# Kernel optimization log

Measured on AMD Instinct MI355X. Metric: run time of the kernel, lower is better.

## Reference

```python
import jax, jax.numpy as jnp
import numpy as np

B, S, HID, HEADS, FF, NL, SPAN, MAXP, VOCAB = 8, 512, 512, 8, 768, 3, 256, 512, 100
DH = HID // HEADS
EPS = 1e-7  # layer_norm_eps
SCALE = float(np.sqrt(DH * 3.0))  # scale_factor = 1 + len(['p2c','c2p']) = 3


def _ln(x, s, b):
    mu = x.mean(-1, keepdims=True)
    var = ((x - mu) ** 2).mean(-1, keepdims=True)
    return (x - mu) / jnp.sqrt(var + EPS) * s + b


def _rel_bucket(seq_len, bucket=SPAN, max_pos=MAXP):
    # DeBERTa-v2 build_relative_position + make_log_bucket_position (static, numpy)
    ids = np.arange(seq_len)
    rel = ids[:, None] - ids[None, :]
    mid = bucket // 2
    abs_pos = np.where((rel < mid) & (rel > -mid), mid - 1, np.abs(rel)).astype(np.float64)
    log_pos = np.ceil(np.log(abs_pos / mid) / np.log((max_pos - 1) / mid) * (mid - 1)) + mid
    bucket_pos = np.where(abs_pos <= mid, rel.astype(np.float64), log_pos * np.sign(rel))
    return jnp.asarray(bucket_pos.astype(np.int32))  # [S, S]


def setup_inputs():
    key = jax.random.key(0)
    ks = jax.random.split(key, 12)
    w = lambda k, shape: jax.random.normal(k, shape, jnp.float32) * 0.02
    return {
        'image_embeddings': jax.random.normal(ks[0], (B, S, HID), jnp.float32),
        'attention_mask': jnp.ones((B, S), jnp.float32),
        'emb_ln_s': jnp.ones((HID,), jnp.float32), 'emb_ln_b': jnp.zeros((HID,), jnp.float32),
        'rel_emb': w(ks[1], (2 * SPAN, HID)),
        'rel_ln_s': jnp.ones((HID,), jnp.float32), 'rel_ln_b': jnp.zeros((HID,), jnp.float32),
        'Wq': w(ks[2], (NL, HID, HID)), 'bq': jnp.zeros((NL, HID), jnp.float32),
        'Wk': w(ks[3], (NL, HID, HID)), 'bk': jnp.zeros((NL, HID), jnp.float32),
        'Wv': w(ks[4], (NL, HID, HID)), 'bv': jnp.zeros((NL, HID), jnp.float32),
        'Wo': w(ks[5], (NL, HID, HID)), 'bo': jnp.zeros((NL, HID), jnp.float32),
        'attn_ln_s': jnp.ones((NL, HID), jnp.float32), 'attn_ln_b': jnp.zeros((NL, HID), jnp.float32),
        'Wi': w(ks[6], (NL, HID, FF)), 'bi': jnp.zeros((NL, FF), jnp.float32),
        'Wf': w(ks[7], (NL, FF, HID)), 'bf': jnp.zeros((NL, HID), jnp.float32),
        'ffn_ln_s': jnp.ones((NL, HID), jnp.float32), 'ffn_ln_b': jnp.zeros((NL, HID), jnp.float32),
        'Wc': w(ks[8], (HID, VOCAB)), 'bc': jnp.zeros((VOCAB,), jnp.float32),
    }


def reference(image_embeddings, attention_mask, emb_ln_s, emb_ln_b, rel_emb, rel_ln_s, rel_ln_b,
              Wq, bq, Wk, bk, Wv, bv, Wo, bo, attn_ln_s, attn_ln_b,
              Wi, bi, Wf, bf, ffn_ln_s, ffn_ln_b, Wc, bc):
    b, s, hid = image_embeddings.shape
    rel = _rel_bucket(s)
    c2p_idx = jnp.clip(rel + SPAN, 0, 2 * SPAN - 1)[None, None]   # [1,1,S,S]
    p2c_idx = jnp.clip(-rel + SPAN, 0, 2 * SPAN - 1)[None, None]  # [1,1,S,S]

    # embeddings: LayerNorm(inputs_embeds) * mask (position_biased_input=False)
    h = _ln(image_embeddings, emb_ln_s, emb_ln_b) * attention_mask[:, :, None]
    rel_e = _ln(rel_emb, rel_ln_s, rel_ln_b)  # norm_rel_ebd='layer_norm'
    m = (attention_mask[:, None, :, None] * attention_mask[:, None, None, :]) > 0  # [B,1,S,S]
    neg = jnp.finfo(h.dtype).min

    for l in range(NL):
        q = (h @ Wq[l] + bq[l]).reshape(b, s, HEADS, DH)
        k = (h @ Wk[l] + bk[l]).reshape(b, s, HEADS, DH)
        v = (h @ Wv[l] + bv[l]).reshape(b, s, HEADS, DH)
        scores = jnp.einsum('bqhd,bkhd->bhqk', q, k) / SCALE
        # share_att_key=True: pos projections reuse key/query projections
        pk = (rel_e @ Wk[l] + bk[l]).reshape(2 * SPAN, HEADS, DH)
        pq = (rel_e @ Wq[l] + bq[l]).reshape(2 * SPAN, HEADS, DH)
        # content-to-position
        c2p = jnp.einsum('bqhd,rhd->bhqr', q, pk)  # [B,H,S,2*SPAN]
        c2p = jnp.take_along_axis(c2p, c2p_idx, axis=-1)  # [B,H,S,S]
        # position-to-content (gather along last dim, then transpose q/k)
        p2c = jnp.einsum('bkhd,rhd->bhkr', k, pq)  # [B,H,S,2*SPAN]
        p2c = jnp.take_along_axis(p2c, p2c_idx, axis=-1).transpose(0, 1, 3, 2)  # [B,H,S,S]
        scores = scores + c2p / SCALE + p2c / SCALE
        # XSoftmax: mask -> -inf, softmax, re-zero masked probs
        probs = jax.nn.softmax(jnp.where(m, scores, neg), axis=-1)
        probs = jnp.where(m, probs, 0.0)
        ctx = jnp.einsum('bhqk,bkhd->bqhd', probs, v).reshape(b, s, hid)
        h = _ln(ctx @ Wo[l] + bo[l] + h, attn_ln_s[l], attn_ln_b[l])
        f = jax.nn.gelu(h @ Wi[l] + bi[l], approximate=False)
        h = _ln(f @ Wf[l] + bf[l] + h, ffn_ln_s[l], ffn_ln_b[l])

    return h @ Wc + bc  # token-classification logits [B,S,VOCAB]
```

## Files before the change

### kernel.cpp

```cpp
#include <hip/hip_runtime.h>
#include <hip/hip_bf16.h>
#include <math.h>

#define EPS_LN 1e-7f
#define INV_SCALE 0.072168783648703221f
#define NEGMAX -3.402823466e38f

typedef unsigned short u16;
typedef __attribute__((ext_vector_type(8))) short bf16x8;
typedef __attribute__((ext_vector_type(4))) float f32x4;

__device__ __forceinline__ u16 f2b(float f) {
  union { float f; unsigned int u; } v; v.f = f;
  unsigned int r = v.u + 0x7FFFu + ((v.u >> 16) & 1u);
  return (u16)(r >> 16);
}
__device__ __forceinline__ float b2f(u16 u) {
  union { unsigned int u; float f; } v; v.u = ((unsigned int)u) << 16;
  return v.f;
}
__device__ __forceinline__ float gelu_exact(float v) {
  return 0.5f * v * (1.f + erff(v * 0.70710678118654752440f));
}
__device__ __forceinline__ int bucket_clip(int rel) {
  int a = (rel < 128 && rel > -128) ? 127 : (rel < 0 ? -rel : rel);
  int bucket;
  if (a <= 128) {
    bucket = rel;
  } else {
    double lp = ceil(log((double)a / 128.0) / log(511.0 / 128.0) * 127.0) + 128.0;
    int l = (int)lp;
    bucket = (rel > 0) ? l : -l;
  }
  int c = bucket + 256;
  return c < 0 ? 0 : (c > 511 ? 511 : c);
}

__global__ __launch_bounds__(256) void relbucket_kernel(int* __restrict__ crel) {
  int idx = blockIdx.x * 256 + threadIdx.x;
  if (idx >= 1023) return;
  crel[idx] = bucket_clip(idx - 511);
}

__global__ __launch_bounds__(256) void biascat_kernel(const float* __restrict__ bq,
                                                      const float* __restrict__ bk,
                                                      const float* __restrict__ bv,
                                                      float* __restrict__ o) {
  int i = blockIdx.x * 256 + threadIdx.x;
  if (i >= 4608) return;
  int l = i / 1536, c = i - l * 1536;
  float v = (c < 512) ? bq[l * 512 + c]
                      : (c < 1024) ? bk[l * 512 + c - 512] : bv[l * 512 + c - 1024];
  o[i] = v;
}

template <bool RESID, bool MASK>
__global__ __launch_bounds__(256) void ln_kernel(const float* __restrict__ x,
                                                 const float* __restrict__ res,
                                                 const float* __restrict__ gam,
                                                 const float* __restrict__ bet,
                                                 const float* __restrict__ mask,
                                                 float* __restrict__ out,
                                                 u16* __restrict__ outb, int nrows) {
  int w = threadIdx.x >> 6, ln = threadIdx.x & 63;
  int row = blockIdx.x * 4 + w;
  if (row >= nrows) return;
  const float* xr = x + (size_t)row * 512;
  float v[8];
#pragma unroll
  for (int c = 0; c < 2; ++c) {
    float4 a = *(const float4*)(xr + (ln << 3) + (c << 2));
    v[c * 4 + 0] = a.x; v[c * 4 + 1] = a.y; v[c * 4 + 2] = a.z; v[c * 4 + 3] = a.w;
    if (RESID) {
      float4 r4 = *(const float4*)(res + (size_t)row * 512 + (ln << 3) + (c << 2));
      v[c * 4 + 0] += r4.x; v[c * 4 + 1] += r4.y; v[c * 4 + 2] += r4.z; v[c * 4 + 3] += r4.w;
    }
  }
  float sum = 0.f;
#pragma unroll
  for (int c = 0; c < 8; ++c) sum += v[c];
#pragma unroll
  for (int off = 32; off; off >>= 1) sum += __shfl_xor(sum, off);
  float mu = sum * (1.f / 512.f);
  float vs = 0.f;
#pragma unroll
  for (int c = 0; c < 8; ++c) { float d = v[c] - mu; vs += d * d; }
#pragma unroll
  for (int off = 32; off; off >>= 1) vs += __shfl_xor(vs, off);
  float rstd = 1.f / sqrtf(vs * (1.f / 512.f) + EPS_LN);
  float mk = MASK ? mask[row] : 1.f;
  float* orow = out + (size_t)row * 512;
  u16* brow = outb ? outb + (size_t)row * 512 : nullptr;
#pragma unroll
  for (int c = 0; c < 2; ++c) {
    int col = (ln << 3) + (c << 2);
    float o[4];
#pragma unroll
    for (int q = 0; q < 4; ++q)
      o[q] = ((v[c * 4 + q] - mu) * rstd * gam[col + q] + bet[col + q]) * mk;
    *(float4*)(orow + col) = make_float4(o[0], o[1], o[2], o[3]);
    if (brow) {
      ushort4 ob = { f2b(o[0]), f2b(o[1]), f2b(o[2]), f2b(o[3]) };
      *(ushort4*)(brow + col) = ob;
    }
  }
}

__global__ __launch_bounds__(256) void wtrans_kernel(const float* __restrict__ W,
                                                     u16* __restrict__ Wt,
                                                     int K, int N, long wstride, long tstride) {
  __shared__ float tl[32][33];
  int z = blockIdx.z;
  W += (size_t)z * wstride;
  Wt += (size_t)z * tstride;
  int n0 = blockIdx.x * 32, k0 = blockIdx.y * 32;
  int c = threadIdx.x & 31, r8 = threadIdx.x >> 5;
#pragma unroll
  for (int p = 0; p < 4; ++p) {
    int r = r8 + p * 8;
    int k = k0 + r, n = n0 + c;
    tl[r][c] = (k < K && n < N) ? W[(size_t)k * N + n] : 0.f;
  }
  __syncthreads();
#pragma unroll
  for (int p = 0; p < 4; ++p) {
    int r = r8 + p * 8;
    int n = n0 + r, k = k0 + c;
    if (n < N && k < K) Wt[(size_t)n * K + k] = f2b(tl[c][r]);
  }
}

__global__ __launch_bounds__(256) void vtrans_kernel(const u16* __restrict__ qkv,
                                                     u16* __restrict__ vT) {
  __shared__ u16 tl[32][33];
  int z = blockIdx.z;
  int b = z >> 3, h = z & 7;
  int j0 = blockIdx.x * 32, d0 = blockIdx.y * 32;
  int c = threadIdx.x & 31, r8 = threadIdx.x >> 5;
#pragma unroll
  for (int p = 0; p < 4; ++p) {
    int r = r8 + p * 8;
    tl[r][c] = qkv[(size_t)(b * 512 + j0 + r) * 1536 + 1024 + h * 64 + d0 + c];
  }
  __syncthreads();
#pragma unroll
  for (int p = 0; p < 4; ++p) {
    int r = r8 + p * 8;
    vT[(size_t)z * 32768 + (size_t)(d0 + r) * 512 + j0 + c] = tl[c][r];
  }
}

template <int EPI, typename CT>
__global__ __launch_bounds__(256) void gemm128(const u16* __restrict__ A,
                                               const u16* __restrict__ B,
                                               const float* __restrict__ bias,
                                               CT* __restrict__ C,
                                               int M, int N, int K,
                                               int lda, int ldb, int ldc) {
  __shared__ u16 As[128][72];
  __shared__ u16 Bs[64][72];
  int t = threadIdx.x;
  int m0 = blockIdx.y * 128, n0 = blockIdx.x * 64;
  int w = t >> 6, l = t & 63;
  int wr = w >> 1, wc = w & 1, lr = l & 15, kg = l >> 4;
  f32x4 acc[4][2] = {};
  for (int k0 = 0; k0 < K; k0 += 64) {
#pragma unroll
    for (int p = 0; p < 4; ++p) {
      int c = t + (p << 8);
      int row = c >> 3, q = c & 7;
      *(uint4*)(&As[row][q * 8]) =
          *(const uint4*)(A + (size_t)(m0 + row) * lda + k0 + q * 8);
    }
#pragma unroll
    for (int p = 0; p < 2; ++p) {
      int c = t + (p << 8);
      int row = c >> 3, q = c & 7;
      *(uint4*)(&Bs[row][q * 8]) =
          *(const uint4*)(B + (size_t)(n0 + row) * ldb + k0 + q * 8);
    }
    __syncthreads();
#pragma unroll
    for (int s = 0; s < 2; ++s) {
      bf16x8 a[4], bb[2];
#pragma unroll
      for (int m = 0; m < 4; ++m)
        a[m] = *(const bf16x8*)(&As[wr * 64 + m * 16 + lr][kg * 8 + s * 32]);
#pragma unroll
      for (int n = 0; n < 2; ++n)
        bb[n] = *(const bf16x8*)(&Bs[wc * 32 + n * 16 + lr][kg * 8 + s * 32]);
#pragma unroll
      for (int m = 0; m < 4; ++m)
#pragma unroll
        for (int n = 0; n < 2; ++n)
          acc[m][n] = __builtin_amdgcn_mfma_f32_16x16x32_bf16(a[m], bb[n], acc[m][n], 0, 0, 0);
    }
    __syncthreads();
  }
#pragma unroll
  for (int m = 0; m < 4; ++m)
#pragma unroll
    for (int n = 0; n < 2; ++n) {
      int col = n0 + wc * 32 + n * 16 + lr;
      float bv = (EPI >= 1) ? bias[col] : 0.f;
#pragma unroll
      for (int r = 0; r < 4; ++r) {
        int row = m0 + wr * 64 + m * 16 + kg * 4 + r;
        float v = acc[m][n][r] + bv;
        if (EPI == 2) v = gelu_exact(v);
        if constexpr (sizeof(CT) == 2) {
          ((u16*)C)[(size_t)row * ldc + col] = f2b(v);
        } else {
          ((float*)C)[(size_t)row * ldc + col] = v;
        }
      }
    }
}

template <int EPI, typename CT>
__global__ __launch_bounds__(256) void gemm_bf16(const u16* __restrict__ A,
                                                 const u16* __restrict__ B,
                                                 const float* __restrict__ bias,
                                                 CT* __restrict__ C,
                                                 int M, int N, int K,
                                                 int lda, int ldb, int ldc) {
  __shared__ u16 As[64][72];
  __shared__ u16 Bs[64][72];
  int t = threadIdx.x;
  int m0 = blockIdx.y * 64, n0 = blockIdx.x * 64;
  int w = t >> 6, l = t & 63;
  int wr = w >> 1, wc = w & 1, lr = l & 15, kg = l >> 4;
  f32x4 acc[2][2] = {};
  for (int k0 = 0; k0 < K; k0 += 64) {
#pragma unroll
    for (int p = 0; p < 2; ++p) {
      int c = t + (p << 8);
      int row = c >> 3, q = c & 7;
      uint4 av = *(const uint4*)(A + (size_t)(m0 + row) * lda + k0 + q * 8);
      *(uint4*)(&As[row][q * 8]) = av;
      uint4 bv = make_uint4(0u, 0u, 0u, 0u);
      if (n0 + row < N) bv = *(const uint4*)(B + (size_t)(n0 + row) * ldb + k0 + q * 8);
      *(uint4*)(&Bs[row][q * 8]) = bv;
    }
    __syncthreads();
#pragma unroll
    for (int s = 0; s < 2; ++s) {
      bf16x8 a0 = *(const bf16x8*)(&As[wr * 32 + lr][kg * 8 + s * 32]);
      bf16x8 a1 = *(const bf16x8*)(&As[wr * 32 + 16 + lr][kg * 8 + s * 32]);
      bf16x8 b0 = *(const bf16x8*)(&Bs[wc * 32 + lr][kg * 8 + s * 32]);
      bf16x8 b1 = *(const bf16x8*)(&Bs[wc * 32 + 16 + lr][kg * 8 + s * 32]);
      acc[0][0] = __builtin_amdgcn_mfma_f32_16x16x32_bf16(a0, b0, acc[0][0], 0, 0, 0);
      acc[0][1] = __builtin_amdgcn_mfma_f32_16x16x32_bf16(a0, b1, acc[0][1], 0, 0, 0);
      acc[1][0] = __builtin_amdgcn_mfma_f32_16x16x32_bf16(a1, b0, acc[1][0], 0, 0, 0);
      acc[1][1] = __builtin_amdgcn_mfma_f32_16x16x32_bf16(a1, b1, acc[1][1], 0, 0, 0);
    }
    __syncthreads();
  }
#pragma unroll
  for (int m = 0; m < 2; ++m)
#pragma unroll
    for (int n = 0; n < 2; ++n) {
      int col = n0 + wc * 32 + n * 16 + lr;
      if (col < N) {
        float bv = (EPI >= 1) ? bias[col] : 0.f;
#pragma unroll
        for (int r = 0; r < 4; ++r) {
          int row = m0 + wr * 32 + m * 16 + kg * 4 + r;
          float v = acc[m][n][r] + bv;
          if (EPI == 2) v = gelu_exact(v);
          if constexpr (sizeof(CT) == 2) {
            ((u16*)C)[(size_t)row * ldc + col] = f2b(v);
          } else {
            ((float*)C)[(size_t)row * ldc + col] = v;
          }
        }
      }
    }
}

__global__ __launch_bounds__(256) void attn_fused(const u16* __restrict__ qkv,
                                                  const u16* __restrict__ vT,
                                                  const float* __restrict__ mask,
                                                  const int* __restrict__ crel,
                                                  u16* __restrict__ po,
                                                  float* __restrict__ pms) {
  __shared__ u16 ks[64][72];
  __shared__ u16 U1[128][72];
  __shared__ u16 U2[128][72];
  __shared__ u16 crl16[1024];
  int t = threadIdx.x;
  int wg = blockIdx.x;
  int xcd = wg & 7, q = wg >> 3;
  int z = xcd * 8 + (q >> 6);
  int rem = q & 63;
  int it = rem >> 3, js = rem & 7;
  int b = z >> 3, h = z & 7;
  int i0 = it * 64, j0 = js * 64;
  int w = t >> 6, l = t & 63;
  int lr = l & 15, kg = l >> 4;

  int ib = bucket_clip(i0 - j0 - 63);

  for (int c = t; c < 1023; c += 256) crl16[c] = (u16)crel[c];
  for (int c = t; c < 512; c += 256) {
    int row = c >> 3, off = (c & 7) * 8;
    *(uint4*)(&ks[row][off]) =
        *(const uint4*)(qkv + (size_t)(b * 512 + j0 + row) * 1536 + 512 + h * 64 + off);
  }
  for (int c = t; c < 1024; c += 256) {
    int row = c >> 3, off = (c & 7) * 8;
    int rw = ib + row;
    rw = rw > 511 ? 511 : rw;
    const u16* relrow = qkv + (size_t)(4096 + rw) * 1536 + h * 64;
    *(uint4*)(&U1[row][off]) = *(const uint4*)(relrow + 512 + off);
    *(uint4*)(&U2[row][off]) = *(const uint4*)(relrow + off);
  }

  const u16* qrow = qkv + (size_t)(b * 512 + i0 + w * 16 + lr) * 1536 + h * 64;
  bf16x8 qa0 = *(const bf16x8*)(qrow + kg * 8);
  bf16x8 qa1 = *(const bf16x8*)(qrow + kg * 8 + 32);
  __syncthreads();

  f32x4 sc[4];
#pragma unroll
  for (int nf = 0; nf < 4; ++nf) {
    bf16x8 kb0 = *(const bf16x8*)(&ks[nf * 16 + lr][kg * 8]);
    bf16x8 kb1 = *(const bf16x8*)(&ks[nf * 16 + lr][kg * 8 + 32]);
    f32x4 a = {};
    a = __builtin_amdgcn_mfma_f32_16x16x32_bf16(qa0, kb0, a, 0, 0, 0);
    a = __builtin_amdgcn_mfma_f32_16x16x32_bf16(qa1, kb1, a, 0, 0, 0);
    sc[nf] = a;
  }
  f32x4 b1a[8];
#pragma unroll
  for (int f = 0; f < 8; ++f) {
    bf16x8 p0 = *(const bf16x8*)(&U1[f * 16 + lr][kg * 8]);
    bf16x8 p1 = *(const bf16x8*)(&U1[f * 16 + lr][kg * 8 + 32]);
    f32x4 a = {};
    a = __builtin_amdgcn_mfma_f32_16x16x32_bf16(qa0, p0, a, 0, 0, 0);
    a = __builtin_amdgcn_mfma_f32_16x16x32_bf16(qa1, p1, a, 0, 0, 0);
    b1a[f] = a;
  }
  f32x4 b2a[2][4];
#pragma unroll
  for (int g = 0; g < 2; ++g) {
    bf16x8 a0 = *(const bf16x8*)(&U2[w * 32 + g * 16 + lr][kg * 8]);
    bf16x8 a1 = *(const bf16x8*)(&U2[w * 32 + g * 16 + lr][kg * 8 + 32]);
#pragma unroll
    for (int f = 0; f < 4; ++f) {
      bf16x8 kb0 = *(const bf16x8*)(&ks[f * 16 + lr][kg * 8]);
      bf16x8 kb1 = *(const bf16x8*)(&ks[f * 16 + lr][kg * 8 + 32]);
      f32x4 a = {};
      a = __builtin_amdgcn_mfma_f32_16x16x32_bf16(a0, kb0, a, 0, 0, 0);
      a = __builtin_amdgcn_mfma_f32_16x16x32_bf16(a1, kb1, a, 0, 0, 0);
      b2a[g][f] = a;
    }
  }
  __syncthreads();
  u16* b1 = &U1[0][0];
#pragma unroll
  for (int f = 0; f < 8; ++f)
#pragma unroll
    for (int r = 0; r < 4; ++r)
      b1[(w * 16 + kg * 4 + r) * 136 + f * 16 + lr] = f2b(b1a[f][r]);
#pragma unroll
  for (int g = 0; g < 2; ++g)
#pragma unroll
    for (int f = 0; f < 4; ++f)
#pragma unroll
      for (int r = 0; r < 4; ++r)
        U2[w * 32 + g * 16 + kg * 4 + r][f * 16 + lr] = f2b(b2a[g][f][r]);
  __syncthreads();

  bf16x8 vb[4][2];
#pragma unroll
  for (int nf = 0; nf < 4; ++nf) {
    const u16* vrow = vT + (size_t)z * 32768 + (size_t)(nf * 16 + lr) * 512 + j0;
    vb[nf][0] = *(const bf16x8*)(vrow + kg * 8);
    vb[nf][1] = *(const bf16x8*)(vrow + kg * 8 + 32);
  }

  float mi[4], mj[4];
#pragma unroll
  for (int r = 0; r < 4; ++r) mi[r] = mask[b * 512 + i0 + w * 16 + kg * 4 + r];
#pragma unroll
  for (int nf = 0; nf < 4; ++nf) mj[nf] = mask[b * 512 + j0 + nf * 16 + lr];
  float lgv[4][4];
  bool ok[4][4];
  float tmax[4] = {NEGMAX, NEGMAX, NEGMAX, NEGMAX};
  int iloc = w * 16 + kg * 4;
#pragma unroll
  for (int nf = 0; nf < 4; ++nf) {
    int jloc = nf * 16 + lr;
    int relc = i0 + iloc - (j0 + jloc) + 511;
#pragma unroll
    for (int r = 0; r < 4; ++r) {
      int idx = crl16[relc + r] - ib;
      float bias = b2f(b1[(iloc + r) * 136 + idx]) + b2f(U2[idx][jloc]);
      bool o_ = (mi[r] * mj[nf]) > 0.f;
      float v = o_ ? (sc[nf][r] + bias) * INV_SCALE : NEGMAX;
      ok[nf][r] = o_;
      lgv[nf][r] = v;
      tmax[r] = fmaxf(tmax[r], v);
    }
  }
#pragma unroll
  for (int r = 0; r < 4; ++r) {
#pragma unroll
    for (int off = 8; off; off >>= 1) tmax[r] = fmaxf(tmax[r], __shfl_xor(tmax[r], off));
  }
  float tsum[4];
#pragma unroll
  for (int r = 0; r < 4; ++r) {
    float mn = tmax[r];
    float ls = 0.f;
#pragma unroll
    for (int nf = 0; nf < 4; ++nf) {
      float p = ok[nf][r] ? __expf(lgv[nf][r] - mn) : 0.f;
      lgv[nf][r] = p;
      ls += p;
    }
    tsum[r] = ls;
  }
#pragma unroll
  for (int r = 0; r < 4; ++r) {
#pragma unroll
    for (int off = 8; off; off >>= 1) tsum[r] += __shfl_xor(tsum[r], off);
  }
#pragma unroll
  for (int nf = 0; nf < 4; ++nf)
#pragma unroll
    for (int r = 0; r < 4; ++r) ks[w * 16 + kg * 4 + r][nf * 16 + lr] = f2b(lgv[nf][r]);
  bf16x8 pa0 = *(const bf16x8*)(&ks[w * 16 + lr][kg * 8]);
  bf16x8 pa1 = *(const bf16x8*)(&ks[w * 16 + lr][kg * 8 + 32]);
  f32x4 o[4] = {};
#pragma unroll
  for (int nf = 0; nf < 4; ++nf) {
    o[nf] = __builtin_amdgcn_mfma_f32_16x16x32_bf16(pa0, vb[nf][0], o[nf], 0, 0, 0);
    o[nf] = __builtin_amdgcn_mfma_f32_16x16x32_bf16(pa1, vb[nf][1], o[nf], 0, 0, 0);
  }
#pragma unroll
  for (int r = 0; r < 4; ++r) {
    int i = i0 + w * 16 + kg * 4 + r;
    size_t pb = (((size_t)js * 64 + z) * 512 + i) * 64;
#pragma unroll
    for (int nf = 0; nf < 4; ++nf) po[pb + nf * 16 + lr] = f2b(o[nf][r]);
    if (lr == 0) {
      size_t mb = (((size_t)js * 64 + z) * 512 + i) * 2;
      pms[mb + 0] = tmax[r];
      pms[mb + 1] = tsum[r];
    }
  }
}

__global__ __launch_bounds__(256) void merge_kernel(const u16* __restrict__ po,
                                                    const float* __restrict__ pms,
                                                    u16* __restrict__ ctx) {
  int t = threadIdx.x;
  int w = t >> 6, d = t & 63;
  int row = blockIdx.x * 4 + w;
  int z = row >> 9, i = row & 511;
  int b = z >> 3, h = z & 7;
  float mv[8], sv[8], m = NEGMAX;
#pragma unroll
  for (int js = 0; js < 8; ++js) {
    size_t mb = (((size_t)js * 64 + z) * 512 + i) * 2;
    mv[js] = pms[mb + 0];
    sv[js] = pms[mb + 1];
    m = fmaxf(m, mv[js]);
  }
  float o = 0.f, s = 0.f;
#pragma unroll
  for (int js = 0; js < 8; ++js) {
    float wgt = (mv[js] <= -1e37f) ? 0.f : __expf(mv[js] - m);
    o += wgt * b2f(po[(((size_t)js * 64 + z) * 512 + i) * 64 + d]);
    s += wgt * sv[js];
  }
  float r = (s > 0.f) ? o / s : 0.f;
  ctx[(size_t)(b * 512 + i) * 512 + h * 64 + d] = f2b(r);
}

extern "C" void kernel_launch(void* const* d_in, const int* in_sizes, int n_in,
                              void* d_out, int out_size, void* d_ws, size_t ws_size,
                              hipStream_t stream) {
  const float* x       = (const float*)d_in[0];
  const float* mask    = (const float*)d_in[1];
  const float* emb_s   = (const float*)d_in[2];
  const float* emb_b   = (const float*)d_in[3];
  const float* rel_emb = (const float*)d_in[4];
  const float* rel_s   = (const float*)d_in[5];
  const float* rel_b   = (const float*)d_in[6];
  const float* Wq = (const float*)d_in[7];
  const float* bq = (const float*)d_in[8];
  const float* Wk = (const float*)d_in[9];
  const float* bk = (const float*)d_in[10];
  const float* Wv = (const float*)d_in[11];
  const float* bv = (const float*)d_in[12];
  const float* Wo = (const float*)d_in[13];
  const float* bo = (const float*)d_in[14];
  const float* as_ = (const float*)d_in[15];
  const float* ab_ = (const float*)d_in[16];
  const float* Wi = (const float*)d_in[17];
  const float* bi = (const float*)d_in[18];
  const float* Wf = (const float*)d_in[19];
  const float* bf_ = (const float*)d_in[20];
  const float* fs_ = (const float*)d_in[21];
  const float* fb_ = (const float*)d_in[22];
  const float* Wc = (const float*)d_in[23];
  const float* bc = (const float*)d_in[24];
  float* out = (float*)d_out;

  char* p = (char*)d_ws;
  auto alloc = [&](size_t bytes) {
    char* r = p;
    p += (bytes + 255) & ~(size_t)255;
    return r;
  };
  float* hcat = (float*)alloc((size_t)4608 * 512 * 4);
  float* tmpA = (float*)alloc((size_t)4096 * 512 * 4);
  u16* mid  = (u16*)alloc((size_t)4096 * 768 * 2);
  u16* hbf  = (u16*)alloc((size_t)4608 * 512 * 2);
  u16* qkv  = (u16*)alloc((size_t)4608 * 1536 * 2);
  u16* vT   = (u16*)alloc((size_t)64 * 64 * 512 * 2);
  u16* ctxb = (u16*)alloc((size_t)4096 * 512 * 2);
  u16* po   = (u16*)alloc((size_t)8 * 64 * 512 * 64 * 2);
  float* pms = (float*)alloc((size_t)8 * 64 * 512 * 2 * 4);
  u16* WtQKV = (u16*)alloc((size_t)3 * 1536 * 512 * 2);
  u16* WtO  = (u16*)alloc((size_t)3 * 512 * 512 * 2);
  u16* WtI  = (u16*)alloc((size_t)3 * 768 * 512 * 2);
  u16* WtF  = (u16*)alloc((size_t)3 * 512 * 768 * 2);
  u16* WtC  = (u16*)alloc((size_t)100 * 512 * 2);
  float* bqkv = (float*)alloc((size_t)3 * 1536 * 4);
  int* crel = (int*)alloc((size_t)1024 * 4);

  relbucket_kernel<<<4, 256, 0, stream>>>(crel);
  biascat_kernel<<<18, 256, 0, stream>>>(bq, bk, bv, bqkv);
  wtrans_kernel<<<dim3(16, 16, 3), 256, 0, stream>>>(Wq, WtQKV, 512, 512, 262144, 786432);
  wtrans_kernel<<<dim3(16, 16, 3), 256, 0, stream>>>(Wk, WtQKV + 262144, 512, 512, 262144, 786432);
  wtrans_kernel<<<dim3(16, 16, 3), 256, 0, stream>>>(Wv, WtQKV + 524288, 512, 512, 262144, 786432);
  wtrans_kernel<<<dim3(16, 16, 3), 256, 0, stream>>>(Wo, WtO, 512, 512, 262144, 262144);
  wtrans_kernel<<<dim3(24, 16, 3), 256, 0, stream>>>(Wi, WtI, 512, 768, 393216, 393216);
  wtrans_kernel<<<dim3(16, 24, 3), 256, 0, stream>>>(Wf, WtF, 768, 512, 393216, 393216);
  wtrans_kernel<<<dim3(4, 16, 1), 256, 0, stream>>>(Wc, WtC, 512, 100, 0, 0);
  ln_kernel<false, true><<<1024, 256, 0, stream>>>(x, nullptr, emb_s, emb_b, mask,
                                                   hcat, hbf, 4096);
  ln_kernel<false, false><<<128, 256, 0, stream>>>(rel_emb, nullptr, rel_s, rel_b, nullptr,
                                                   hcat + (size_t)4096 * 512,
                                                   hbf + (size_t)4096 * 512, 512);

  for (int l = 0; l < 3; ++l) {
    gemm128<1, u16><<<dim3(24, 36), 256, 0, stream>>>(
        hbf, WtQKV + (size_t)l * 786432, bqkv + l * 1536, qkv,
        4608, 1536, 512, 512, 512, 1536);
    vtrans_kernel<<<dim3(16, 2, 64), 256, 0, stream>>>(qkv, vT);
    attn_fused<<<4096, 256, 0, stream>>>(qkv, vT, mask, crel, po, pms);
    merge_kernel<<<8192, 256, 0, stream>>>(po, pms, ctxb);
    gemm128<1, float><<<dim3(8, 32), 256, 0, stream>>>(
        ctxb, WtO + (size_t)l * 262144, bo + l * 512, tmpA, 4096, 512, 512, 512, 512, 512);
    ln_kernel<true, false><<<1024, 256, 0, stream>>>(tmpA, hcat, as_ + l * 512, ab_ + l * 512,
                                                     nullptr, hcat, hbf, 4096);
    gemm128<2, u16><<<dim3(12, 32), 256, 0, stream>>>(
        hbf, WtI + (size_t)l * 393216, bi + l * 768, mid, 4096, 768, 512, 512, 512, 768);
    gemm128<1, float><<<dim3(8, 32), 256, 0, stream>>>(
        mid, WtF + (size_t)l * 393216, bf_ + l * 512, tmpA, 4096, 512, 768, 768, 768, 512);
    ln_kernel<true, false><<<1024, 256, 0, stream>>>(tmpA, hcat, fs_ + l * 512, fb_ + l * 512,
                                                     nullptr, hcat, hbf, 4096);
  }
  gemm_bf16<1, float><<<dim3(2, 64), 256, 0, stream>>>(
      hbf, WtC, bc, out, 4096, 100, 512, 512, 512, 100);
}
```

Measured before the change: 473.9 us.

## Fuse setup kernels, V-transpose into QKV GEMM, trim attention bias tiles

Merges the bucket-table and bias-concat kernels into one launch and the seven weight-transpose launches into one. The V transpose now happens in the QKV GEMM epilogue, which removes the separate vtrans kernel. In the attention kernel, K fragments are loaded straight into registers instead of shared memory. Only the relative-position rows actually spanned by each tile (F fragments) are loaded and multiplied. Softmax uses exp2 with a prescaled log2e factor, and partial outputs are written in a packed fragment layout that the merge kernel reads back with new indexing. The extra epilogue stores slow the QKV GEMM somewhat, and the lost per-launch overlap costs a little, in exchange for fewer launches and less attention work.

```diff
diff --git a/kernel.cpp b/kernel.cpp
--- a/kernel.cpp
+++ b/kernel.cpp
@@ -36,22 +36,20 @@
   return c < 0 ? 0 : (c > 511 ? 511 : c);
 }
 
-__global__ __launch_bounds__(256) void relbucket_kernel(int* __restrict__ crel) {
-  int idx = blockIdx.x * 256 + threadIdx.x;
-  if (idx >= 1023) return;
-  crel[idx] = bucket_clip(idx - 511);
-}
-
-__global__ __launch_bounds__(256) void biascat_kernel(const float* __restrict__ bq,
-                                                      const float* __restrict__ bk,
-                                                      const float* __restrict__ bv,
-                                                      float* __restrict__ o) {
+__global__ __launch_bounds__(256) void tables_kernel(const float* __restrict__ bq,
+                                                     const float* __restrict__ bk,
+                                                     const float* __restrict__ bv,
+                                                     int* __restrict__ crel,
+                                                     float* __restrict__ bqkv) {
   int i = blockIdx.x * 256 + threadIdx.x;
-  if (i >= 4608) return;
-  int l = i / 1536, c = i - l * 1536;
-  float v = (c < 512) ? bq[l * 512 + c]
-                      : (c < 1024) ? bk[l * 512 + c - 512] : bv[l * 512 + c - 1024];
-  o[i] = v;
+  if (i < 1023) crel[i] = bucket_clip(i - 511);
+  int j = i - 1024;
+  if (j >= 0 && j < 4608) {
+    int l = j / 1536, c = j - l * 1536;
+    float v = (c < 512) ? bq[l * 512 + c]
+                        : (c < 1024) ? bk[l * 512 + c - 512] : bv[l * 512 + c - 1024];
+    bqkv[j] = v;
+  }
 }
 
 template <bool RESID, bool MASK>
@@ -106,14 +104,40 @@
   }
 }
 
-__global__ __launch_bounds__(256) void wtrans_kernel(const float* __restrict__ W,
-                                                     u16* __restrict__ Wt,
-                                                     int K, int N, long wstride, long tstride) {
+__global__ __launch_bounds__(256) void wtrans_all(const float* __restrict__ Wq,
+                                                  const float* __restrict__ Wk,
+                                                  const float* __restrict__ Wv,
+                                                  const float* __restrict__ Wo,
+                                                  const float* __restrict__ Wi,
+                                                  const float* __restrict__ Wf,
+                                                  const float* __restrict__ Wc,
+                                                  u16* __restrict__ WtQKV,
+                                                  u16* __restrict__ WtO,
+                                                  u16* __restrict__ WtI,
+                                                  u16* __restrict__ WtF,
+                                                  u16* __restrict__ WtC) {
   __shared__ float tl[32][33];
-  int z = blockIdx.z;
-  W += (size_t)z * wstride;
-  Wt += (size_t)z * tstride;
+  int job = blockIdx.z;
+  const float* W; u16* Wt; int K, N;
+  if (job < 9) {
+    int l = job / 3, p3 = job % 3;
+    W = (p3 == 0 ? Wq : p3 == 1 ? Wk : Wv) + (size_t)l * 262144;
+    Wt = WtQKV + (size_t)l * 786432 + (size_t)p3 * 262144;
+    K = 512; N = 512;
+  } else if (job < 12) {
+    int l = job - 9; W = Wo + (size_t)l * 262144; Wt = WtO + (size_t)l * 262144;
+    K = 512; N = 512;
+  } else if (job < 15) {
+    int l = job - 12; W = Wi + (size_t)l * 393216; Wt = WtI + (size_t)l * 393216;
+    K = 512; N = 768;
+  } else if (job < 18) {
+    int l = job - 15; W = Wf + (size_t)l * 393216; Wt = WtF + (size_t)l * 393216;
+    K = 768; N = 512;
+  } else {
+    W = Wc; Wt = WtC; K = 512; N = 100;
+  }
   int n0 = blockIdx.x * 32, k0 = blockIdx.y * 32;
+  if (n0 >= N || k0 >= K) return;
   int c = threadIdx.x & 31, r8 = threadIdx.x >> 5;
 #pragma unroll
   for (int p = 0; p < 4; ++p) {
@@ -130,33 +154,14 @@
   }
 }
 
-__global__ __launch_bounds__(256) void vtrans_kernel(const u16* __restrict__ qkv,
-                                                     u16* __restrict__ vT) {
-  __shared__ u16 tl[32][33];
-  int z = blockIdx.z;
-  int b = z >> 3, h = z & 7;
-  int j0 = blockIdx.x * 32, d0 = blockIdx.y * 32;
-  int c = threadIdx.x & 31, r8 = threadIdx.x >> 5;
-#pragma unroll
-  for (int p = 0; p < 4; ++p) {
-    int r = r8 + p * 8;
-    tl[r][c] = qkv[(size_t)(b * 512 + j0 + r) * 1536 + 1024 + h * 64 + d0 + c];
-  }
-  __syncthreads();
-#pragma unroll
-  for (int p = 0; p < 4; ++p) {
-    int r = r8 + p * 8;
-    vT[(size_t)z * 32768 + (size_t)(d0 + r) * 512 + j0 + c] = tl[c][r];
-  }
-}
-
-template <int EPI, typename CT>
+template <int EPI, int VT, typename CT>
 __global__ __launch_bounds__(256) void gemm128(const u16* __restrict__ A,
                                                const u16* __restrict__ B,
                                                const float* __restrict__ bias,
                                                CT* __restrict__ C,
                                                int M, int N, int K,
-                                               int lda, int ldb, int ldc) {
+                                               int lda, int ldb, int ldc,
+                                               u16* __restrict__ vTout) {
   __shared__ u16 As[128][72];
   __shared__ u16 Bs[64][72];
   int t = threadIdx.x;
@@ -203,15 +208,25 @@
     for (int n = 0; n < 2; ++n) {
       int col = n0 + wc * 32 + n * 16 + lr;
       float bv = (EPI >= 1) ? bias[col] : 0.f;
+      int rowb = m0 + wr * 64 + m * 16 + kg * 4;
+      float vv[4];
 #pragma unroll
       for (int r = 0; r < 4; ++r) {
-        int row = m0 + wr * 64 + m * 16 + kg * 4 + r;
         float v = acc[m][n][r] + bv;
         if (EPI == 2) v = gelu_exact(v);
+        vv[r] = v;
         if constexpr (sizeof(CT) == 2) {
-          ((u16*)C)[(size_t)row * ldc + col] = f2b(v);
+          ((u16*)C)[(size_t)(rowb + r) * ldc + col] = f2b(v);
         } else {
-          ((float*)C)[(size_t)row * ldc + col] = v;
+          ((float*)C)[(size_t)(rowb + r) * ldc + col] = v;
+        }
+      }
+      if (VT) {
+        if (col >= 1024 && rowb < 4096) {
+          int zz = (rowb >> 9) * 8 + ((col - 1024) >> 6);
+          int dd = (col - 1024) & 63;
+          ushort4 o4 = { f2b(vv[0]), f2b(vv[1]), f2b(vv[2]), f2b(vv[3]) };
+          *(ushort4*)(vTout + (size_t)zz * 32768 + (size_t)dd * 512 + (rowb & 511)) = o4;
         }
       }
     }
@@ -284,15 +299,14 @@
                                                   const int* __restrict__ crel,
                                                   u16* __restrict__ po,
                                                   float* __restrict__ pms) {
-  __shared__ u16 ks[64][72];
   __shared__ u16 U1[128][72];
   __shared__ u16 U2[128][72];
   __shared__ u16 crl16[1024];
   int t = threadIdx.x;
   int wg = blockIdx.x;
-  int xcd = wg & 7, q = wg >> 3;
-  int z = xcd * 8 + (q >> 6);
-  int rem = q & 63;
+  int xcd = wg & 7, qq = wg >> 3;
+  int z = xcd * 8 + (qq >> 6);
+  int rem = qq & 63;
   int it = rem >> 3, js = rem & 7;
   int b = z >> 3, h = z & 7;
   int i0 = it * 64, j0 = js * 64;
@@ -300,14 +314,11 @@
   int lr = l & 15, kg = l >> 4;
 
   int ib = bucket_clip(i0 - j0 - 63);
+  int ie = bucket_clip(i0 - j0 + 63);
+  int F = (ie - ib + 16) >> 4;
 
   for (int c = t; c < 1023; c += 256) crl16[c] = (u16)crel[c];
-  for (int c = t; c < 512; c += 256) {
-    int row = c >> 3, off = (c & 7) * 8;
-    *(uint4*)(&ks[row][off]) =
-        *(const uint4*)(qkv + (size_t)(b * 512 + j0 + row) * 1536 + 512 + h * 64 + off);
-  }
-  for (int c = t; c < 1024; c += 256) {
+  for (int c = t; c < F * 128; c += 256) {
     int row = c >> 3, off = (c & 7) * 8;
     int rw = ib + row;
     rw = rw > 511 ? 511 : rw;
@@ -315,61 +326,75 @@
     *(uint4*)(&U1[row][off]) = *(const uint4*)(relrow + 512 + off);
     *(uint4*)(&U2[row][off]) = *(const uint4*)(relrow + off);
   }
-
   const u16* qrow = qkv + (size_t)(b * 512 + i0 + w * 16 + lr) * 1536 + h * 64;
   bf16x8 qa0 = *(const bf16x8*)(qrow + kg * 8);
   bf16x8 qa1 = *(const bf16x8*)(qrow + kg * 8 + 32);
+  bf16x8 kb[4][2];
+#pragma unroll
+  for (int nf = 0; nf < 4; ++nf) {
+    const u16* krow = qkv + (size_t)(b * 512 + j0 + nf * 16 + lr) * 1536 + 512 + h * 64;
+    kb[nf][0] = *(const bf16x8*)(krow + kg * 8);
+    kb[nf][1] = *(const bf16x8*)(krow + kg * 8 + 32);
+  }
   __syncthreads();
 
   f32x4 sc[4];
 #pragma unroll
   for (int nf = 0; nf < 4; ++nf) {
-    bf16x8 kb0 = *(const bf16x8*)(&ks[nf * 16 + lr][kg * 8]);
-    bf16x8 kb1 = *(const bf16x8*)(&ks[nf * 16 + lr][kg * 8 + 32]);
     f32x4 a = {};
-    a = __builtin_amdgcn_mfma_f32_16x16x32_bf16(qa0, kb0, a, 0, 0, 0);
-    a = __builtin_amdgcn_mfma_f32_16x16x32_bf16(qa1, kb1, a, 0, 0, 0);
+    a = __builtin_amdgcn_mfma_f32_16x16x32_bf16(qa0, kb[nf][0], a, 0, 0, 0);
+    a = __builtin_amdgcn_mfma_f32_16x16x32_bf16(qa1, kb[nf][1], a, 0, 0, 0);
     sc[nf] = a;
   }
-  f32x4 b1a[8];
+  f32x4 b1a[8] = {};
 #pragma unroll
   for (int f = 0; f < 8; ++f) {
-    bf16x8 p0 = *(const bf16x8*)(&U1[f * 16 + lr][kg * 8]);
-    bf16x8 p1 = *(const bf16x8*)(&U1[f * 16 + lr][kg * 8 + 32]);
-    f32x4 a = {};
-    a = __builtin_amdgcn_mfma_f32_16x16x32_bf16(qa0, p0, a, 0, 0, 0);
-    a = __builtin_amdgcn_mfma_f32_16x16x32_bf16(qa1, p1, a, 0, 0, 0);
-    b1a[f] = a;
-  }
-  f32x4 b2a[2][4];
+    if (f < F) {
+      bf16x8 p0 = *(const bf16x8*)(&U1[f * 16 + lr][kg * 8]);
+      bf16x8 p1 = *(const bf16x8*)(&U1[f * 16 + lr][kg * 8 + 32]);
+      f32x4 a = {};
+      a = __builtin_amdgcn_mfma_f32_16x16x32_bf16(qa0, p0, a, 0, 0, 0);
+      a = __builtin_amdgcn_mfma_f32_16x16x32_bf16(qa1, p1, a, 0, 0, 0);
+      b1a[f] = a;
+    }
+  }
+  f32x4 b2a[2][4] = {};
 #pragma unroll
   for (int g = 0; g < 2; ++g) {
-    bf16x8 a0 = *(const bf16x8*)(&U2[w * 32 + g * 16 + lr][kg * 8]);
-    bf16x8 a1 = *(const bf16x8*)(&U2[w * 32 + g * 16 + lr][kg * 8 + 32]);
-#pragma unroll
-    for (int f = 0; f < 4; ++f) {
-      bf16x8 kb0 = *(const bf16x8*)(&ks[f * 16 + lr][kg * 8]);
-      bf16x8 kb1 = *(const bf16x8*)(&ks[f * 16 + lr][kg * 8 + 32]);
-      f32x4 a = {};
-      a = __builtin_amdgcn_mfma_f32_16x16x32_bf16(a0, kb0, a, 0, 0, 0);
-      a = __builtin_amdgcn_mfma_f32_16x16x32_bf16(a1, kb1, a, 0, 0, 0);
-      b2a[g][f] = a;
+    int fr = w + g * 4;
+    if (fr < F) {
+      bf16x8 a0 = *(const bf16x8*)(&U2[fr * 16 + lr][kg * 8]);
+      bf16x8 a1 = *(const bf16x8*)(&U2[fr * 16 + lr][kg * 8 + 32]);
+#pragma unroll
+      for (int nf = 0; nf < 4; ++nf) {
+        f32x4 a = {};
+        a = __builtin_amdgcn_mfma_f32_16x16x32_bf16(a0, kb[nf][0], a, 0, 0, 0);
+        a = __builtin_amdgcn_mfma_f32_16x16x32_bf16(a1, kb[nf][1], a, 0, 0, 0);
+        b2a[g][nf] = a;
+      }
     }
   }
   __syncthreads();
   u16* b1 = &U1[0][0];
 #pragma unroll
-  for (int f = 0; f < 8; ++f)
-#pragma unroll
-    for (int r = 0; r < 4; ++r)
-      b1[(w * 16 + kg * 4 + r) * 136 + f * 16 + lr] = f2b(b1a[f][r]);
-#pragma unroll
-  for (int g = 0; g < 2; ++g)
-#pragma unroll
-    for (int f = 0; f < 4; ++f)
+  for (int f = 0; f < 8; ++f) {
+    if (f < F) {
 #pragma unroll
       for (int r = 0; r < 4; ++r)
-        U2[w * 32 + g * 16 + kg * 4 + r][f * 16 + lr] = f2b(b2a[g][f][r]);
+        b1[(w * 16 + kg * 4 + r) * 136 + f * 16 + lr] = f2b(b1a[f][r]);
+    }
+  }
+#pragma unroll
+  for (int g = 0; g < 2; ++g) {
+    int fr = w + g * 4;
+    if (fr < F) {
+#pragma unroll
+      for (int nf = 0; nf < 4; ++nf)
+#pragma unroll
+        for (int r = 0; r < 4; ++r)
+          U2[fr * 16 + kg * 4 + r][nf * 16 + lr] = f2b(b2a[g][nf][r]);
+    }
+  }
   __syncthreads();
 
   bf16x8 vb[4][2];
@@ -380,6 +405,7 @@
     vb[nf][1] = *(const bf16x8*)(vrow + kg * 8 + 32);
   }
 
+  const float SC2 = INV_SCALE * 1.4426950408889634f;
   float mi[4], mj[4];
 #pragma unroll
   for (int r = 0; r < 4; ++r) mi[r] = mask[b * 512 + i0 + w * 16 + kg * 4 + r];
@@ -398,7 +424,7 @@
       int idx = crl16[relc + r] - ib;
       float bias = b2f(b1[(iloc + r) * 136 + idx]) + b2f(U2[idx][jloc]);
       bool o_ = (mi[r] * mj[nf]) > 0.f;
-      float v = o_ ? (sc[nf][r] + bias) * INV_SCALE : NEGMAX;
+      float v = o_ ? (sc[nf][r] + bias) * SC2 : NEGMAX;
       ok[nf][r] = o_;
       lgv[nf][r] = v;
       tmax[r] = fmaxf(tmax[r], v);
@@ -416,7 +442,7 @@
     float ls = 0.f;
 #pragma unroll
     for (int nf = 0; nf < 4; ++nf) {
-      float p = ok[nf][r] ? __expf(lgv[nf][r] - mn) : 0.f;
+      float p = ok[nf][r] ? exp2f(lgv[nf][r] - mn) : 0.f;
       lgv[nf][r] = p;
       ls += p;
     }
@@ -427,25 +453,33 @@
 #pragma unroll
     for (int off = 8; off; off >>= 1) tsum[r] += __shfl_xor(tsum[r], off);
   }
+  __syncthreads();
+  u16 (*ps)[16][72] = (u16(*)[16][72]) & U1[0][0];
 #pragma unroll
   for (int nf = 0; nf < 4; ++nf)
 #pragma unroll
-    for (int r = 0; r < 4; ++r) ks[w * 16 + kg * 4 + r][nf * 16 + lr] = f2b(lgv[nf][r]);
-  bf16x8 pa0 = *(const bf16x8*)(&ks[w * 16 + lr][kg * 8]);
-  bf16x8 pa1 = *(const bf16x8*)(&ks[w * 16 + lr][kg * 8 + 32]);
+    for (int r = 0; r < 4; ++r) ps[w][kg * 4 + r][nf * 16 + lr] = f2b(lgv[nf][r]);
+  bf16x8 pa0 = *(const bf16x8*)(&ps[w][lr][kg * 8]);
+  bf16x8 pa1 = *(const bf16x8*)(&ps[w][lr][kg * 8 + 32]);
   f32x4 o[4] = {};
 #pragma unroll
   for (int nf = 0; nf < 4; ++nf) {
     o[nf] = __builtin_amdgcn_mfma_f32_16x16x32_bf16(pa0, vb[nf][0], o[nf], 0, 0, 0);
     o[nf] = __builtin_amdgcn_mfma_f32_16x16x32_bf16(pa1, vb[nf][1], o[nf], 0, 0, 0);
   }
+  unsigned int pk[8];
+#pragma unroll
+  for (int nf = 0; nf < 4; ++nf) {
+    pk[nf * 2 + 0] = (unsigned int)f2b(o[nf][0]) | ((unsigned int)f2b(o[nf][1]) << 16);
+    pk[nf * 2 + 1] = (unsigned int)f2b(o[nf][2]) | ((unsigned int)f2b(o[nf][3]) << 16);
+  }
+  size_t base = (((((size_t)js * 64 + z) * 8 + it) * 4 + w) * 64 + l) * 16;
+  *(uint4*)(po + base) = make_uint4(pk[0], pk[1], pk[2], pk[3]);
+  *(uint4*)(po + base + 8) = make_uint4(pk[4], pk[5], pk[6], pk[7]);
 #pragma unroll
   for (int r = 0; r < 4; ++r) {
-    int i = i0 + w * 16 + kg * 4 + r;
-    size_t pb = (((size_t)js * 64 + z) * 512 + i) * 64;
-#pragma unroll
-    for (int nf = 0; nf < 4; ++nf) po[pb + nf * 16 + lr] = f2b(o[nf][r]);
     if (lr == 0) {
+      int i = i0 + w * 16 + kg * 4 + r;
       size_t mb = (((size_t)js * 64 + z) * 512 + i) * 2;
       pms[mb + 0] = tmax[r];
       pms[mb + 1] = tsum[r];
@@ -457,10 +491,13 @@
                                                     const float* __restrict__ pms,
                                                     u16* __restrict__ ctx) {
   int t = threadIdx.x;
-  int w = t >> 6, d = t & 63;
-  int row = blockIdx.x * 4 + w;
+  int w_ = t >> 6, d = t & 63;
+  int row = blockIdx.x * 4 + w_;
   int z = row >> 9, i = row & 511;
   int b = z >> 3, h = z & 7;
+  int it = i >> 6, ii = i & 63;
+  int aw = ii >> 4, akg = (ii >> 2) & 3, ar = ii & 3;
+  int alr = d & 15, anf = d >> 4;
   float mv[8], sv[8], m = NEGMAX;
 #pragma unroll
   for (int js = 0; js < 8; ++js) {
@@ -472,8 +509,10 @@
   float o = 0.f, s = 0.f;
 #pragma unroll
   for (int js = 0; js < 8; ++js) {
-    float wgt = (mv[js] <= -1e37f) ? 0.f : __expf(mv[js] - m);
-    o += wgt * b2f(po[(((size_t)js * 64 + z) * 512 + i) * 64 + d]);
+    float wgt = (mv[js] <= -1e37f) ? 0.f : exp2f(mv[js] - m);
+    size_t pb = (((((size_t)js * 64 + z) * 8 + it) * 4 + aw) * 64 + (akg * 16 + alr)) * 16
+                + anf * 4 + ar;
+    o += wgt * b2f(po[pb]);
     s += wgt * sv[js];
   }
   float r = (s > 0.f) ? o / s : 0.f;
@@ -533,15 +572,9 @@
   float* bqkv = (float*)alloc((size_t)3 * 1536 * 4);
   int* crel = (int*)alloc((size_t)1024 * 4);
 
-  relbucket_kernel<<<4, 256, 0, stream>>>(crel);
-  biascat_kernel<<<18, 256, 0, stream>>>(bq, bk, bv, bqkv);
-  wtrans_kernel<<<dim3(16, 16, 3), 256, 0, stream>>>(Wq, WtQKV, 512, 512, 262144, 786432);
-  wtrans_kernel<<<dim3(16, 16, 3), 256, 0, stream>>>(Wk, WtQKV + 262144, 512, 512, 262144, 786432);
-  wtrans_kernel<<<dim3(16, 16, 3), 256, 0, stream>>>(Wv, WtQKV + 524288, 512, 512, 262144, 786432);
-  wtrans_kernel<<<dim3(16, 16, 3), 256, 0, stream>>>(Wo, WtO, 512, 512, 262144, 262144);
-  wtrans_kernel<<<dim3(24, 16, 3), 256, 0, stream>>>(Wi, WtI, 512, 768, 393216, 393216);
-  wtrans_kernel<<<dim3(16, 24, 3), 256, 0, stream>>>(Wf, WtF, 768, 512, 393216, 393216);
-  wtrans_kernel<<<dim3(4, 16, 1), 256, 0, stream>>>(Wc, WtC, 512, 100, 0, 0);
+  tables_kernel<<<22, 256, 0, stream>>>(bq, bk, bv, crel, bqkv);
+  wtrans_all<<<dim3(24, 24, 19), 256, 0, stream>>>(Wq, Wk, Wv, Wo, Wi, Wf, Wc,
+                                                   WtQKV, WtO, WtI, WtF, WtC);
   ln_kernel<false, true><<<1024, 256, 0, stream>>>(x, nullptr, emb_s, emb_b, mask,
                                                    hcat, hbf, 4096);
   ln_kernel<false, false><<<128, 256, 0, stream>>>(rel_emb, nullptr, rel_s, rel_b, nullptr,
@@ -549,20 +582,22 @@
                                                    hbf + (size_t)4096 * 512, 512);
 
   for (int l = 0; l < 3; ++l) {
-    gemm128<1, u16><<<dim3(24, 36), 256, 0, stream>>>(
+    gemm128<1, 1, u16><<<dim3(24, 36), 256, 0, stream>>>(
         hbf, WtQKV + (size_t)l * 786432, bqkv + l * 1536, qkv,
-        4608, 1536, 512, 512, 512, 1536);
-    vtrans_kernel<<<dim3(16, 2, 64), 256, 0, stream>>>(qkv, vT);
+        4608, 1536, 512, 512, 512, 1536, vT);
     attn_fused<<<4096, 256, 0, stream>>>(qkv, vT, mask, crel, po, pms);
     merge_kernel<<<8192, 256, 0, stream>>>(po, pms, ctxb);
-    gemm128<1, float><<<dim3(8, 32), 256, 0, stream>>>(
-        ctxb, WtO + (size_t)l * 262144, bo + l * 512, tmpA, 4096, 512, 512, 512, 512, 512);
+    gemm128<1, 0, float><<<dim3(8, 32), 256, 0, stream>>>(
+        ctxb, WtO + (size_t)l * 262144, bo + l * 512, tmpA, 4096, 512, 512,
+        512, 512, 512, nullptr);
     ln_kernel<true, false><<<1024, 256, 0, stream>>>(tmpA, hcat, as_ + l * 512, ab_ + l * 512,
                                                      nullptr, hcat, hbf, 4096);
-    gemm128<2, u16><<<dim3(12, 32), 256, 0, stream>>>(
-        hbf, WtI + (size_t)l * 393216, bi + l * 768, mid, 4096, 768, 512, 512, 512, 768);
-    gemm128<1, float><<<dim3(8, 32), 256, 0, stream>>>(
-        mid, WtF + (size_t)l * 393216, bf_ + l * 512, tmpA, 4096, 512, 768, 768, 768, 512);
+    gemm128<2, 0, u16><<<dim3(12, 32), 256, 0, stream>>>(
+        hbf, WtI + (size_t)l * 393216, bi + l * 768, mid, 4096, 768, 512,
+        512, 512, 768, nullptr);
+    gemm128<1, 0, float><<<dim3(8, 32), 256, 0, stream>>>(
+        mid, WtF + (size_t)l * 393216, bf_ + l * 512, tmpA, 4096, 512, 768,
+        768, 768, 512, nullptr);
     ln_kernel<true, false><<<1024, 256, 0, stream>>>(tmpA, hcat, fs_ + l * 512, fb_ + l * 512,
                                                      nullptr, hcat, hbf, 4096);
   }
```

Measured after the change: 792.6 us. +67.2%, slower.
